# Kernel optimization log

Hardware: AMD Instinct MI355X
Metric: run time of the kernel (lower is better)

Reference implementation:

```python
import jax, jax.numpy as jnp
import numpy as np

N = 50000      # nodes
EPS = 1e-5     # BatchNorm eps


def setup_inputs() -> dict:
    key = jax.random.key(0)
    ks = jax.random.split(key, 8)
    F_IN, H, C, E = 128, 128, 40, 600000
    x = jax.random.normal(ks[0], (N, F_IN), jnp.float32)
    edge_index = jax.random.randint(ks[1], (2, E), 0, N, dtype=jnp.int64)
    def glorot(k, fi, fo):
        s = np.sqrt(6.0 / (fi + fo)).astype(np.float32)
        return jax.random.uniform(k, (fi, fo), jnp.float32, -s, s)
    return {
        "x": x, "edge_index": edge_index,
        "W1": glorot(ks[2], F_IN, H), "b1": jnp.zeros((H,), jnp.float32),
        "gamma1": jnp.ones((H,), jnp.float32), "beta1": jnp.zeros((H,), jnp.float32),
        "W2": glorot(ks[3], H, H), "b2": jnp.zeros((H,), jnp.float32),
        "gamma2": jnp.ones((H,), jnp.float32), "beta2": jnp.zeros((H,), jnp.float32),
        "W3": glorot(ks[4], H, C), "b3": jnp.zeros((C,), jnp.float32),
    }


def _gcn_conv(x, W, b, src, dst, norm):
    # X' = D^-1/2 (A+I) D^-1/2 (X W) + b   (PyG GCNConv with self-loops)
    h = x @ W                               # [N, Fo]
    msg = h[src] * norm[:, None]            # [E+N, Fo] gather + scale
    out = jax.ops.segment_sum(msg, dst, num_segments=N)  # scatter-add
    return out + b


def _batchnorm(x, gamma, beta):
    # training-mode BatchNorm1d: batch stats over node axis, biased variance
    mu = jnp.mean(x, axis=0)
    var = jnp.mean(jnp.square(x - mu), axis=0)
    return (x - mu) * jax.lax.rsqrt(var + EPS) * gamma + beta


def reference(x, edge_index, W1, b1, gamma1, beta1, W2, b2, gamma2, beta2, W3, b3):
    loops = jnp.arange(N, dtype=edge_index.dtype)
    src = jnp.concatenate([edge_index[0], loops])
    dst = jnp.concatenate([edge_index[1], loops])
    deg = jax.ops.segment_sum(jnp.ones_like(dst, dtype=x.dtype), dst, num_segments=N)
    dinv = jax.lax.rsqrt(jnp.maximum(deg, 1.0))  # deg >= 1 due to self-loops
    norm = dinv[src] * dinv[dst]                 # [E+N]

    h = _gcn_conv(x, W1, b1, src, dst, norm)
    h = jax.nn.relu(_batchnorm(h, gamma1, beta1))
    h = _gcn_conv(h, W2, b2, src, dst, norm)
    h = jax.nn.relu(_batchnorm(h, gamma2, beta2))
    h = _gcn_conv(h, W3, b3, src, dst, norm)
    return jax.nn.log_softmax(h, axis=-1)
```

## Files before the change

### kernel.cpp

```cpp
#include <hip/hip_runtime.h>
#include <hip/hip_bf16.h>

#define EPS 1e-5f
#define SCAN_BLOCKS 256

typedef __attribute__((ext_vector_type(8))) short bf16x8;
typedef __attribute__((ext_vector_type(4))) float f32x4;

__device__ inline float bf2f(unsigned short u) {
    union { unsigned int i; float f; } v;
    v.i = ((unsigned int)u) << 16;
    return v.f;
}

__device__ inline unsigned short f2bf(float f) {
    union { float f; unsigned int i; } v;
    v.f = f;
    unsigned int x = v.i;
    unsigned int rounded = x + 0x7FFF + ((x >> 16) & 1);
    return (unsigned short)(rounded >> 16);
}


__global__ void count_kernel(const int* __restrict__ dst, int* __restrict__ counts, int e) {
    int i = blockIdx.x * blockDim.x + threadIdx.x;
    if (i < e) atomicAdd(&counts[dst[i]], 1);
}

__global__ __launch_bounds__(256) void scan_partial_kernel(const int* __restrict__ counts,
                                                           int* __restrict__ partials, int n) {
    __shared__ int sh[256];
    int chunk = (n + gridDim.x - 1) / gridDim.x;
    int lo = blockIdx.x * chunk;
    int hi = lo + chunk; if (hi > n) hi = n;
    int s = 0;
    for (int i = lo + threadIdx.x; i < hi; i += 256) s += counts[i];
    sh[threadIdx.x] = s;
    __syncthreads();
    for (int d = 128; d; d >>= 1) {
        if (threadIdx.x < d) sh[threadIdx.x] += sh[threadIdx.x + d];
        __syncthreads();
    }
    if (threadIdx.x == 0) partials[blockIdx.x] = sh[0];
}

__global__ __launch_bounds__(256) void scan_level2_kernel(int* __restrict__ partials) {
    __shared__ int sh[256];
    int t = threadIdx.x;
    sh[t] = partials[t];
    __syncthreads();
    for (int d = 1; d < 256; d <<= 1) {
        int v = (t >= d) ? sh[t - d] : 0;
        __syncthreads();
        sh[t] += v;
        __syncthreads();
    }
    partials[t] = (t == 0) ? 0 : sh[t - 1];
}

__global__ __launch_bounds__(256) void scan_write_kernel(const int* __restrict__ counts,
                                                         const int* __restrict__ partials,
                                                         int* __restrict__ offs,
                                                         float* __restrict__ dinv, int n) {
    __shared__ int sh[256];
    int t = threadIdx.x;
    int chunk = (n + gridDim.x - 1) / gridDim.x;
    int lo = blockIdx.x * chunk;
    int hi = lo + chunk; if (hi > n) hi = n;
    int per = (chunk + 255) / 256;
    int tlo = lo + t * per;
    int thi = tlo + per; if (thi > hi) thi = hi;
    int s = 0;
    for (int i = tlo; i < thi; ++i) s += counts[i];
    sh[t] = s;
    __syncthreads();
    for (int d = 1; d < 256; d <<= 1) {
        int v = (t >= d) ? sh[t - d] : 0;
        __syncthreads();
        sh[t] += v;
        __syncthreads();
    }
    int run = partials[blockIdx.x] + ((t == 0) ? 0 : sh[t - 1]);
    for (int i = tlo; i < thi; ++i) {
        offs[i] = run;
        run += counts[i];
        dinv[i] = rsqrtf((float)(counts[i] + 1));
    }
    if (tlo < n && thi == n) offs[n] = run;
}

__global__ void scatter_kernel(const int* __restrict__ src, const int* __restrict__ dst,
                               const int* __restrict__ offs, int* __restrict__ fill,
                               const float* __restrict__ dinv,
                               int2* __restrict__ csr, int e) {
    int i = blockIdx.x * blockDim.x + threadIdx.x;
    if (i >= e) return;
    int s = src[i], d = dst[i];
    int pos = offs[d] + atomicAdd(&fill[d], 1);
    float w = dinv[s] * dinv[d];
    csr[pos] = make_int2(s, __float_as_int(w));
}

__global__ void prep_weights_kernel(const float* __restrict__ W1, const float* __restrict__ W2,
                                    const float* __restrict__ W3,
                                    unsigned short* __restrict__ WT1,
                                    unsigned short* __restrict__ WT2,
                                    unsigned short* __restrict__ WT3) {
    int i = blockIdx.x * blockDim.x + threadIdx.x;
    if (i < 16384) {
        int col = i >> 7, k = i & 127;
        WT1[i] = f2bf(W1[k * 128 + col]);
    } else if (i < 32768) {
        int j = i - 16384;
        int col = j >> 7, k = j & 127;
        WT2[j] = f2bf(W2[k * 128 + col]);
    } else if (i < 32768 + 6144) {
        int j = i - 32768;
        int col = j >> 7, k = j & 127;
        WT3[j] = (col < 40) ? f2bf(W3[k * 40 + col]) : 0;
    }
}

template<int MODE>
__global__ __launch_bounds__(256) void gemm128_mfma_kernel(
    const void* __restrict__ Aptr, const unsigned short* __restrict__ WT,
    const float* __restrict__ stats, const float* __restrict__ gamma,
    const float* __restrict__ beta, float invn,
    unsigned short* __restrict__ C, int n) {
    __shared__ unsigned short lW[128 * 128];
    __shared__ unsigned short lA[64 * 128];
    __shared__ float scs[128], shs[128];
    int tid = threadIdx.x;
    if (MODE == 1) {
        if (tid < 128) {
            float mu = stats[tid] * invn;
            float var = stats[128 + tid] * invn - mu * mu;
            float sc = gamma[tid] * rsqrtf(var + EPS);
            scs[tid] = sc;
            shs[tid] = beta[tid] - mu * sc;
        }
        __syncthreads();
    }
    const uint4* wsrc = (const uint4*)WT;
#pragma unroll
    for (int it = 0; it < 8; ++it) {
        int idx = tid + it * 256;
        int byte = idx << 4;
        int dst = byte ^ (((byte >> 8) & 7) << 4);
        *(uint4*)((char*)lW + dst) = wsrc[idx];
    }
    int row0 = blockIdx.x * 64;
#pragma unroll
    for (int it = 0; it < 4; ++it) {
        int idx = tid + it * 256;
        int r = idx >> 4;
        int cc = (idx & 15) << 3;
        int gr = row0 + r; if (gr > n - 1) gr = n - 1;
        union { unsigned short u[8]; uint4 q; } t;
        if (MODE == 0) {
            const float* ap = (const float*)Aptr + (size_t)gr * 128 + cc;
            float4 f0 = *(const float4*)ap;
            float4 f1 = *(const float4*)(ap + 4);
            float v[8] = {f0.x, f0.y, f0.z, f0.w, f1.x, f1.y, f1.z, f1.w};
#pragma unroll
            for (int j = 0; j < 8; ++j) t.u[j] = f2bf(v[j]);
        } else {
            uint4 q = *(const uint4*)((const unsigned short*)Aptr + (size_t)gr * 128 + cc);
            unsigned int w[4] = {q.x, q.y, q.z, q.w};
#pragma unroll
            for (int j = 0; j < 8; ++j) {
                float x = bf2f((unsigned short)(w[j >> 1] >> ((j & 1) * 16)));
                int c = cc + j;
                x = fmaf(x, scs[c], shs[c]);
                x = x > 0.0f ? x : 0.0f;
                t.u[j] = f2bf(x);
            }
        }
        int byte = idx << 4;
        int dst = byte ^ (((byte >> 8) & 7) << 4);
        *(uint4*)((char*)lA + dst) = t.q;
    }
    __syncthreads();

    int lane = tid & 63;
    int mrow0 = (tid >> 6) << 4;
    int arow = mrow0 + (lane & 15);
    int swz = (lane & 7) << 4;
    int koff = (lane >> 4) << 4;
    const char* pA = (const char*)lA + (arow << 8);
    const char* pB = (const char*)lW + ((lane & 15) << 8);
    f32x4 acc[8];
#pragma unroll
    for (int t8 = 0; t8 < 8; ++t8) acc[t8] = (f32x4){0.f, 0.f, 0.f, 0.f};
#pragma unroll
    for (int kk = 0; kk < 4; ++kk) {
        int kb = (kk << 6) + koff;
        bf16x8 af = *(const bf16x8*)(pA + (kb ^ swz));
#pragma unroll
        for (int t8 = 0; t8 < 8; ++t8) {
            bf16x8 bf = *(const bf16x8*)(pB + (t8 << 12) + (kb ^ swz));
            acc[t8] = __builtin_amdgcn_mfma_f32_16x16x32_bf16(af, bf, acc[t8], 0, 0, 0);
        }
    }
    int crow = row0 + mrow0 + ((lane >> 4) << 2);
    int ccol = lane & 15;
    unsigned short* cp = C + (size_t)crow * 128 + ccol;
#pragma unroll
    for (int j = 0; j < 4; ++j) {
        if (crow + j < n) {
#pragma unroll
            for (int t8 = 0; t8 < 8; ++t8)
                cp[(size_t)j * 128 + t8 * 16] = f2bf(acc[t8][j]);
        }
    }
}

__global__ __launch_bounds__(256) void gemm40_lsm_mfma_kernel(
    const unsigned short* __restrict__ A, const unsigned short* __restrict__ WT,
    const float* __restrict__ b3, float* __restrict__ out, int n) {
    __shared__ unsigned short lW[48 * 128];
    __shared__ unsigned short lA[64 * 128];
    __shared__ float sRow[64 * 49];
    __shared__ float sD[64];
    __shared__ float sB[48];
    int tid = threadIdx.x;
    if (tid < 48) sB[tid] = (tid < 40) ? b3[tid] : 0.0f;
    const uint4* wsrc = (const uint4*)WT;
#pragma unroll
    for (int it = 0; it < 3; ++it) {
        int idx = tid + it * 256;
        int byte = idx << 4;
        int dst = byte ^ (((byte >> 8) & 7) << 4);
        *(uint4*)((char*)lW + dst) = wsrc[idx];
    }
    int row0 = blockIdx.x * 64;
#pragma unroll
    for (int it = 0; it < 4; ++it) {
        int idx = tid + it * 256;
        int r = idx >> 4;
        int cc = (idx & 15) << 3;
        int gr = row0 + r; if (gr > n - 1) gr = n - 1;
        uint4 q = *(const uint4*)(A + (size_t)gr * 128 + cc);
        int byte = idx << 4;
        int dst = byte ^ (((byte >> 8) & 7) << 4);
        *(uint4*)((char*)lA + dst) = q;
    }
    __syncthreads();

    int lane = tid & 63;
    int mrow0 = (tid >> 6) << 4;
    int arow = mrow0 + (lane & 15);
    int swz = (lane & 7) << 4;
    int koff = (lane >> 4) << 4;
    const char* pA = (const char*)lA + (arow << 8);
    const char* pB = (const char*)lW + ((lane & 15) << 8);
    f32x4 acc[3];
#pragma unroll
    for (int t8 = 0; t8 < 3; ++t8) acc[t8] = (f32x4){0.f, 0.f, 0.f, 0.f};
#pragma unroll
    for (int kk = 0; kk < 4; ++kk) {
        int kb = (kk << 6) + koff;
        bf16x8 af = *(const bf16x8*)(pA + (kb ^ swz));
#pragma unroll
        for (int t8 = 0; t8 < 3; ++t8) {
            bf16x8 bf = *(const bf16x8*)(pB + (t8 << 12) + (kb ^ swz));
            acc[t8] = __builtin_amdgcn_mfma_f32_16x16x32_bf16(af, bf, acc[t8], 0, 0, 0);
        }
    }
    int lrow = mrow0 + ((lane >> 4) << 2);
    int ccol = lane & 15;
#pragma unroll
    for (int t8 = 0; t8 < 3; ++t8)
#pragma unroll
        for (int j = 0; j < 4; ++j)
            sRow[(lrow + j) * 49 + t8 * 16 + ccol] = acc[t8][j] + sB[t8 * 16 + ccol];
    __syncthreads();
    if (tid < 64) {
        float m = -1e30f;
        for (int c = 0; c < 40; ++c) m = fmaxf(m, sRow[tid * 49 + c]);
        float l = 0.0f;
        for (int c = 0; c < 40; ++c) l += expf(sRow[tid * 49 + c] - m);
        sD[tid] = m + logf(l);
    }
    __syncthreads();
    for (int i = tid; i < 64 * 40; i += 256) {
        int r = i / 40;
        int c = i - r * 40;
        int gr = row0 + r;
        if (gr < n) out[(size_t)gr * 40 + c] = sRow[r * 49 + c] - sD[r];
    }
}


template<bool BN>
__global__ __launch_bounds__(256) void aggregate128_kernel(
    const unsigned short* __restrict__ H, const int* __restrict__ offs,
    const int2* __restrict__ csr, const float* __restrict__ dinv,
    const float* __restrict__ stats, const float* __restrict__ gamma,
    const float* __restrict__ beta, float invn,
    unsigned short* __restrict__ out, int n) {
    int node = (blockIdx.x * blockDim.x + threadIdx.x) >> 6;
    if (node >= n) return;
    int lane = threadIdx.x & 63;
    int c0 = lane * 2;
    float sc0 = 1.0f, sh0 = 0.0f, sc1 = 1.0f, sh1 = 0.0f;
    if (BN) {
        float mu0 = stats[c0] * invn;
        float var0 = stats[128 + c0] * invn - mu0 * mu0;
        sc0 = gamma[c0] * rsqrtf(var0 + EPS);
        sh0 = beta[c0] - mu0 * sc0;
        float mu1 = stats[c0 + 1] * invn;
        float var1 = stats[128 + c0 + 1] * invn - mu1 * mu1;
        sc1 = gamma[c0 + 1] * rsqrtf(var1 + EPS);
        sh1 = beta[c0 + 1] - mu1 * sc1;
    }
    auto loadf = [&](int row) -> float2 {
        unsigned int hv = *(const unsigned int*)(H + (size_t)row * 128 + c0);
        float x0 = bf2f((unsigned short)hv);
        float x1 = bf2f((unsigned short)(hv >> 16));
        if (BN) {
            x0 = fmaf(x0, sc0, sh0); x0 = x0 > 0.0f ? x0 : 0.0f;
            x1 = fmaf(x1, sc1, sh1); x1 = x1 > 0.0f ? x1 : 0.0f;
        }
        return make_float2(x0, x1);
    };
    float di = dinv[node];
    float2 self = loadf(node);
    float2 a0 = make_float2(self.x * di * di, self.y * di * di);
    float2 a1 = make_float2(0.f, 0.f), a2 = make_float2(0.f, 0.f), a3 = make_float2(0.f, 0.f);
    int e = offs[node], e1 = offs[node + 1];
    for (; e + 4 <= e1; e += 4) {
        int2 q0 = csr[e], q1 = csr[e + 1], q2 = csr[e + 2], q3 = csr[e + 3];
        float2 h0 = loadf(q0.x);
        float2 h1 = loadf(q1.x);
        float2 h2 = loadf(q2.x);
        float2 h3 = loadf(q3.x);
        float w0 = __int_as_float(q0.y), w1 = __int_as_float(q1.y);
        float w2 = __int_as_float(q2.y), w3 = __int_as_float(q3.y);
        a0.x = fmaf(h0.x, w0, a0.x); a0.y = fmaf(h0.y, w0, a0.y);
        a1.x = fmaf(h1.x, w1, a1.x); a1.y = fmaf(h1.y, w1, a1.y);
        a2.x = fmaf(h2.x, w2, a2.x); a2.y = fmaf(h2.y, w2, a2.y);
        a3.x = fmaf(h3.x, w3, a3.x); a3.y = fmaf(h3.y, w3, a3.y);
    }
    for (; e < e1; ++e) {
        int2 q = csr[e];
        float2 h = loadf(q.x);
        float w = __int_as_float(q.y);
        a0.x = fmaf(h.x, w, a0.x); a0.y = fmaf(h.y, w, a0.y);
    }
    float rx = (a0.x + a1.x) + (a2.x + a3.x);
    float ry = (a0.y + a1.y) + (a2.y + a3.y);
    unsigned int pack = (unsigned int)f2bf(rx) | ((unsigned int)f2bf(ry) << 16);
    *(unsigned int*)(out + (size_t)node * 128 + c0) = pack;
}


__global__ __launch_bounds__(256) void bn_stats_kernel(const unsigned short* __restrict__ X,
                                                       float* __restrict__ stats, int n) {
    int tid = threadIdx.x;
    int c = tid & 127;
    int r0 = blockIdx.x * 2 + (tid >> 7);
    float s = 0.0f, q = 0.0f;
    for (int r = r0; r < n; r += gridDim.x * 2) {
        float v = bf2f(X[(size_t)r * 128 + c]);
        s += v;
        q += v * v;
    }
    __shared__ float sh[256], shq[256];
    sh[tid] = s; shq[tid] = q;
    __syncthreads();
    if (tid < 128) {
        atomicAdd(&stats[c], sh[tid] + sh[tid + 128]);
        atomicAdd(&stats[128 + c], shq[tid] + shq[tid + 128]);
    }
}


extern "C" void kernel_launch(void* const* d_in, const int* in_sizes, int n_in,
                              void* d_out, int out_size, void* d_ws, size_t ws_size,
                              hipStream_t stream) {
    const float* x   = (const float*)d_in[0];
    const int*   ei  = (const int*)d_in[1];
    const float* W1  = (const float*)d_in[2];
    const float* g1  = (const float*)d_in[4];
    const float* bt1 = (const float*)d_in[5];
    const float* W2  = (const float*)d_in[6];
    const float* g2  = (const float*)d_in[8];
    const float* bt2 = (const float*)d_in[9];
    const float* W3  = (const float*)d_in[10];
    const float* b3  = (const float*)d_in[11];

    int n = in_sizes[0] / 128;
    int e = in_sizes[1] / 2;
    const int* src = ei;
    const int* dst = ei + e;

    char* p = (char*)d_ws;
    auto alloc = [&](size_t bytes) -> char* {
        char* q = p;
        p += (bytes + 255) & ~(size_t)255;
        return q;
    };
    int*            counts   = (int*)alloc((size_t)n * 4);
    int*            offs     = (int*)alloc((size_t)(n + 1) * 4);
    int*            fill     = (int*)alloc((size_t)n * 4);
    float*          dinv     = (float*)alloc((size_t)n * 4);
    int*            partials = (int*)alloc(SCAN_BLOCKS * 4);
    int2*           csr      = (int2*)alloc((size_t)e * 8);
    float*          stats    = (float*)alloc(512 * 4);
    unsigned short* WT1      = (unsigned short*)alloc(16384 * 2);
    unsigned short* WT2      = (unsigned short*)alloc(16384 * 2);
    unsigned short* WT3      = (unsigned short*)alloc(6144 * 2);
    unsigned short* Hb       = (unsigned short*)alloc((size_t)n * 128 * 2);
    unsigned short* Ab       = (unsigned short*)alloc((size_t)n * 128 * 2);
    unsigned short* Ab2      = (unsigned short*)alloc((size_t)n * 128 * 2);
    unsigned short* Hb2      = (unsigned short*)alloc((size_t)n * 128 * 2);

    hipMemsetAsync(counts, 0, (size_t)n * 4, stream);
    hipMemsetAsync(fill, 0, (size_t)n * 4, stream);
    hipMemsetAsync(stats, 0, 512 * 4, stream);

    const int tb = 256;
    float invn = 1.0f / n;
    prep_weights_kernel<<<(38912 + tb - 1) / tb, tb, 0, stream>>>(W1, W2, W3, WT1, WT2, WT3);
    count_kernel<<<(e + tb - 1) / tb, tb, 0, stream>>>(dst, counts, e);
    scan_partial_kernel<<<SCAN_BLOCKS, tb, 0, stream>>>(counts, partials, n);
    scan_level2_kernel<<<1, tb, 0, stream>>>(partials);
    scan_write_kernel<<<SCAN_BLOCKS, tb, 0, stream>>>(counts, partials, offs, dinv, n);
    scatter_kernel<<<(e + tb - 1) / tb, tb, 0, stream>>>(src, dst, offs, fill, dinv, csr, e);

    int gblocks = (n + 63) / 64;
    int ablocks = (n + 3) / 4;

    gemm128_mfma_kernel<0><<<gblocks, tb, 0, stream>>>(x, WT1, nullptr, nullptr, nullptr,
                                                       0.0f, Hb, n);
    aggregate128_kernel<false><<<ablocks, tb, 0, stream>>>(Hb, offs, csr, dinv, nullptr,
                                                           nullptr, nullptr, 0.0f, Ab, n);
    bn_stats_kernel<<<256, tb, 0, stream>>>(Ab, stats, n);
    gemm128_mfma_kernel<1><<<gblocks, tb, 0, stream>>>(Ab, WT2, stats, g1, bt1, invn, Hb, n);
    aggregate128_kernel<false><<<ablocks, tb, 0, stream>>>(Hb, offs, csr, dinv, nullptr,
                                                           nullptr, nullptr, 0.0f, Ab2, n);
    bn_stats_kernel<<<256, tb, 0, stream>>>(Ab2, stats + 256, n);
    aggregate128_kernel<true><<<ablocks, tb, 0, stream>>>(Ab2, offs, csr, dinv, stats + 256,
                                                          g2, bt2, invn, Hb2, n);
    gemm40_lsm_mfma_kernel<<<gblocks, tb, 0, stream>>>(Hb2, WT3, b3, (float*)d_out, n);
}
```

Baseline: 269.1 us.

## Fuse BatchNorm statistics into aggregation via grid-stride persistent warps

Removes the separate bn_stats kernels by accumulating per-channel sum and sum-of-squares inside the aggregation kernel, then flushing them with atomics at the end. To keep the atomic count small, the aggregation becomes a fixed grid of 2048 blocks where each wave loops over nodes with a grid stride. This drops one full read of the N x 128 bf16 activation per layer and two launches. The stats are now taken from fp32 values before bf16 rounding, so they differ slightly from before.

After: 971.4 us. +260.9%, slower.

```diff
diff --git a/kernel.cpp b/kernel.cpp
--- a/kernel.cpp
+++ b/kernel.cpp
@@ -292,19 +292,19 @@
 }
 
 
-template<bool BN>
+template<int MODE>
 __global__ __launch_bounds__(256) void aggregate128_kernel(
     const unsigned short* __restrict__ H, const int* __restrict__ offs,
     const int2* __restrict__ csr, const float* __restrict__ dinv,
     const float* __restrict__ stats, const float* __restrict__ gamma,
     const float* __restrict__ beta, float invn,
-    unsigned short* __restrict__ out, int n) {
-    int node = (blockIdx.x * blockDim.x + threadIdx.x) >> 6;
-    if (node >= n) return;
+    unsigned short* __restrict__ out, float* __restrict__ statsOut, int n) {
+    int wid = (blockIdx.x * blockDim.x + threadIdx.x) >> 6;
+    int nw = (gridDim.x * blockDim.x) >> 6;
     int lane = threadIdx.x & 63;
     int c0 = lane * 2;
     float sc0 = 1.0f, sh0 = 0.0f, sc1 = 1.0f, sh1 = 0.0f;
-    if (BN) {
+    if (MODE == 1) {
         float mu0 = stats[c0] * invn;
         float var0 = stats[128 + c0] * invn - mu0 * mu0;
         sc0 = gamma[c0] * rsqrtf(var0 + EPS);
@@ -318,60 +318,54 @@
         unsigned int hv = *(const unsigned int*)(H + (size_t)row * 128 + c0);
         float x0 = bf2f((unsigned short)hv);
         float x1 = bf2f((unsigned short)(hv >> 16));
-        if (BN) {
+        if (MODE == 1) {
             x0 = fmaf(x0, sc0, sh0); x0 = x0 > 0.0f ? x0 : 0.0f;
             x1 = fmaf(x1, sc1, sh1); x1 = x1 > 0.0f ? x1 : 0.0f;
         }
         return make_float2(x0, x1);
     };
-    float di = dinv[node];
-    float2 self = loadf(node);
-    float2 a0 = make_float2(self.x * di * di, self.y * di * di);
-    float2 a1 = make_float2(0.f, 0.f), a2 = make_float2(0.f, 0.f), a3 = make_float2(0.f, 0.f);
-    int e = offs[node], e1 = offs[node + 1];
-    for (; e + 4 <= e1; e += 4) {
-        int2 q0 = csr[e], q1 = csr[e + 1], q2 = csr[e + 2], q3 = csr[e + 3];
-        float2 h0 = loadf(q0.x);
-        float2 h1 = loadf(q1.x);
-        float2 h2 = loadf(q2.x);
-        float2 h3 = loadf(q3.x);
-        float w0 = __int_as_float(q0.y), w1 = __int_as_float(q1.y);
-        float w2 = __int_as_float(q2.y), w3 = __int_as_float(q3.y);
-        a0.x = fmaf(h0.x, w0, a0.x); a0.y = fmaf(h0.y, w0, a0.y);
-        a1.x = fmaf(h1.x, w1, a1.x); a1.y = fmaf(h1.y, w1, a1.y);
-        a2.x = fmaf(h2.x, w2, a2.x); a2.y = fmaf(h2.y, w2, a2.y);
-        a3.x = fmaf(h3.x, w3, a3.x); a3.y = fmaf(h3.y, w3, a3.y);
-    }
-    for (; e < e1; ++e) {
-        int2 q = csr[e];
-        float2 h = loadf(q.x);
-        float w = __int_as_float(q.y);
-        a0.x = fmaf(h.x, w, a0.x); a0.y = fmaf(h.y, w, a0.y);
-    }
-    float rx = (a0.x + a1.x) + (a2.x + a3.x);
-    float ry = (a0.y + a1.y) + (a2.y + a3.y);
-    unsigned int pack = (unsigned int)f2bf(rx) | ((unsigned int)f2bf(ry) << 16);
-    *(unsigned int*)(out + (size_t)node * 128 + c0) = pack;
-}
-
-
-__global__ __launch_bounds__(256) void bn_stats_kernel(const unsigned short* __restrict__ X,
-                                                       float* __restrict__ stats, int n) {
-    int tid = threadIdx.x;
-    int c = tid & 127;
-    int r0 = blockIdx.x * 2 + (tid >> 7);
-    float s = 0.0f, q = 0.0f;
-    for (int r = r0; r < n; r += gridDim.x * 2) {
-        float v = bf2f(X[(size_t)r * 128 + c]);
-        s += v;
-        q += v * v;
-    }
-    __shared__ float sh[256], shq[256];
-    sh[tid] = s; shq[tid] = q;
-    __syncthreads();
-    if (tid < 128) {
-        atomicAdd(&stats[c], sh[tid] + sh[tid + 128]);
-        atomicAdd(&stats[128 + c], shq[tid] + shq[tid + 128]);
+    float s0 = 0.0f, s1 = 0.0f, q0 = 0.0f, q1 = 0.0f;
+    for (int node = wid; node < n; node += nw) {
+        float di = dinv[node];
+        float dd = di * di;
+        float2 self = loadf(node);
+        float2 a0 = make_float2(self.x * dd, self.y * dd);
+        float2 a1 = make_float2(0.f, 0.f), a2 = make_float2(0.f, 0.f),
+               a3 = make_float2(0.f, 0.f);
+        int e = offs[node], e1 = offs[node + 1];
+        for (; e + 4 <= e1; e += 4) {
+            int2 e0v = csr[e], e1v = csr[e + 1], e2v = csr[e + 2], e3v = csr[e + 3];
+            float2 h0 = loadf(e0v.x);
+            float2 h1 = loadf(e1v.x);
+            float2 h2 = loadf(e2v.x);
+            float2 h3 = loadf(e3v.x);
+            float w0 = __int_as_float(e0v.y), w1 = __int_as_float(e1v.y);
+            float w2 = __int_as_float(e2v.y), w3 = __int_as_float(e3v.y);
+            a0.x = fmaf(h0.x, w0, a0.x); a0.y = fmaf(h0.y, w0, a0.y);
+            a1.x = fmaf(h1.x, w1, a1.x); a1.y = fmaf(h1.y, w1, a1.y);
+            a2.x = fmaf(h2.x, w2, a2.x); a2.y = fmaf(h2.y, w2, a2.y);
+            a3.x = fmaf(h3.x, w3, a3.x); a3.y = fmaf(h3.y, w3, a3.y);
+        }
+        for (; e < e1; ++e) {
+            int2 qv = csr[e];
+            float2 h = loadf(qv.x);
+            float w = __int_as_float(qv.y);
+            a0.x = fmaf(h.x, w, a0.x); a0.y = fmaf(h.y, w, a0.y);
+        }
+        float rx = (a0.x + a1.x) + (a2.x + a3.x);
+        float ry = (a0.y + a1.y) + (a2.y + a3.y);
+        if (MODE == 0) {
+            s0 += rx; s1 += ry;
+            q0 = fmaf(rx, rx, q0); q1 = fmaf(ry, ry, q1);
+        }
+        unsigned int pack = (unsigned int)f2bf(rx) | ((unsigned int)f2bf(ry) << 16);
+        *(unsigned int*)(out + (size_t)node * 128 + c0) = pack;
+    }
+    if (MODE == 0) {
+        atomicAdd(&statsOut[c0], s0);
+        atomicAdd(&statsOut[c0 + 1], s1);
+        atomicAdd(&statsOut[128 + c0], q0);
+        atomicAdd(&statsOut[128 + c0 + 1], q1);
     }
 }
 
@@ -430,18 +424,16 @@
     scatter_kernel<<<(e + tb - 1) / tb, tb, 0, stream>>>(src, dst, offs, fill, dinv, csr, e);
 
     int gblocks = (n + 63) / 64;
-    int ablocks = (n + 3) / 4;
+    int ablocks = 2048;
 
     gemm128_mfma_kernel<0><<<gblocks, tb, 0, stream>>>(x, WT1, nullptr, nullptr, nullptr,
                                                        0.0f, Hb, n);
-    aggregate128_kernel<false><<<ablocks, tb, 0, stream>>>(Hb, offs, csr, dinv, nullptr,
-                                                           nullptr, nullptr, 0.0f, Ab, n);
-    bn_stats_kernel<<<256, tb, 0, stream>>>(Ab, stats, n);
+    aggregate128_kernel<0><<<ablocks, tb, 0, stream>>>(Hb, offs, csr, dinv, nullptr, nullptr,
+                                                       nullptr, 0.0f, Ab, stats, n);
     gemm128_mfma_kernel<1><<<gblocks, tb, 0, stream>>>(Ab, WT2, stats, g1, bt1, invn, Hb, n);
-    aggregate128_kernel<false><<<ablocks, tb, 0, stream>>>(Hb, offs, csr, dinv, nullptr,
-                                                           nullptr, nullptr, 0.0f, Ab2, n);
-    bn_stats_kernel<<<256, tb, 0, stream>>>(Ab2, stats + 256, n);
-    aggregate128_kernel<true><<<ablocks, tb, 0, stream>>>(Ab2, offs, csr, dinv, stats + 256,
-                                                          g2, bt2, invn, Hb2, n);
+    aggregate128_kernel<0><<<ablocks, tb, 0, stream>>>(Hb, offs, csr, dinv, nullptr, nullptr,
+                                                       nullptr, 0.0f, Ab2, stats + 256, n);
+    aggregate128_kernel<1><<<ablocks, tb, 0, stream>>>(Ab2, offs, csr, dinv, stats + 256,
+                                                       g2, bt2, invn, Hb2, nullptr, n);
     gemm40_lsm_mfma_kernel<<<gblocks, tb, 0, stream>>>(Hb2, WT3, b3, (float*)d_out, n);
 }
```
